# Performance work log

Measured on AMD Instinct MI355X. Metric: run time of the kernel, lower is better.

## Reference

```python
import jax, jax.numpy as jnp
import numpy as np

MAX_SPAN_LEN = 6

def setup_inputs() -> dict:
    key = jax.random.key(0)
    k1, k2 = jax.random.split(key)
    B, L, H = 16, 1024, 768
    span_adjacency = jax.random.uniform(k1, (B, L, L, 1), dtype=jnp.float32)
    bound_hidden = jax.random.normal(k2, (B, L, H), dtype=jnp.float32)
    return {"span_adjacency": span_adjacency, "bound_hidden": bound_hidden}

def reference(span_adjacency, bound_hidden):
    # out[:, j] = sum_{i=j}^{min(j+6,L)-1} w[:,j,i] * concat(h[:,i], h[:,j])
    B, L, H = bound_hidden.shape
    d = jnp.arange(MAX_SPAN_LEN)                      # window offsets [6]
    j = jnp.arange(L)                                  # [L]
    idx = jnp.minimum(j[:, None] + d[None, :], L - 1)  # [L, 6] clamped gather index
    valid = (j[:, None] + d[None, :]) < L              # [L, 6] window mask
    # gather window weights: w[:, j, j+d] -> [B, L, 6]
    w = span_adjacency[:, j[:, None], idx, 0] * valid.astype(span_adjacency.dtype)
    # gather window hiddens: h[:, j+d] -> [B, L, 6, H]
    h_win = bound_hidden[:, idx]
    first = jnp.einsum('bjd,bjdh->bjh', w, h_win)      # sum_i w * h_i
    wsum = jnp.sum(w, axis=-1, keepdims=True)          # [B, L, 1]
    second = bound_hidden * wsum                       # h_j * sum_i w
    return jnp.concatenate([first, second], axis=-1)   # [B, L, 2H]
```

## Files before the change

kernel.cpp:

```cpp
#include <hip/hip_runtime.h>


#define LROWS 1024
#define HDIM  768
#define SPANW 6
#define HALO  (SPANW - 1)
#define RCHUNK 16
#define CHUNKS (LROWS / RCHUNK)
#define BLK   384

typedef float f32x2 __attribute__((ext_vector_type(2)));

__global__ __launch_bounds__(BLK) void boundary_seg_kernel(
    const float* __restrict__ span,
    const float* __restrict__ bound,
    float* __restrict__ out)
{
    const int tid  = threadIdx.x;
    const int b    = blockIdx.x >> 6;
    const int j0   = (blockIdx.x & (CHUNKS - 1)) * RCHUNK;
    const int bL   = b * LROWS;
    const int colf = tid << 1;

    const float* bcol = bound + (size_t)bL * HDIM + colf;
    f32x2 h[RCHUNK + HALO];
#pragma unroll
    for (int r = 0; r < RCHUNK + HALO; ++r) {
        int gr = j0 + r;
        if (gr > LROWS - 1) gr = LROWS - 1;
        h[r] = *(const f32x2*)(bcol + (size_t)gr * HDIM);
    }

    const float* sdiag = span + (size_t)(bL + j0) * LROWS + j0;

#pragma unroll
    for (int s = 0; s < RCHUNK; ++s) {
        const int j = j0 + s;
        const float* sp = sdiag + (size_t)s * (LROWS + 1);

        float w[SPANW], wsum = 0.f;
#pragma unroll
        for (int d = 0; d < SPANW; ++d) {
            w[d] = (j + d < LROWS) ? sp[d] : 0.f;
            wsum += w[d];
        }

        f32x2 acc = w[0] * h[s]     + w[1] * h[s + 1] + w[2] * h[s + 2]
                  + w[3] * h[s + 3] + w[4] * h[s + 4] + w[5] * h[s + 5];
        const f32x2 sec = h[s] * wsum;

        float* orow = out + (size_t)(bL + j) * (2 * HDIM) + colf;
        *(f32x2*)orow          = acc;
        *(f32x2*)(orow + HDIM) = sec;
    }
}

extern "C" void kernel_launch(void* const* d_in, const int* in_sizes, int n_in,
                              void* d_out, int out_size, void* d_ws, size_t ws_size,
                              hipStream_t stream) {
    const float* span  = (const float*)d_in[0];
    const float* bound = (const float*)d_in[1];
    float* out = (float*)d_out;

    const int B = in_sizes[1] / (LROWS * HDIM);
    dim3 grid(B * CHUNKS), block(BLK);
    hipLaunchKernelGGL(boundary_seg_kernel, grid, block, 0, stream,
                       span, bound, out);
}
```

Measured before the change: 180.9 us.

## Widen to float4 columns, stage span weights in LDS, swizzle workgroups across XCDs

Each thread now handles four columns with 128-bit loads and stores, which halves the block size. The six diagonal span weights per row and their sum are loaded once by 16 threads into shared memory instead of by every thread. Workgroup IDs are remapped so that consecutive chunks land on the same XCD, aiming for better L2 locality on the halo rows. The cost is a barrier, a larger register footprint (21 float4 values), and a launch-bounds occupancy hint.

```diff
diff --git a/kernel.cpp b/kernel.cpp
--- a/kernel.cpp
+++ b/kernel.cpp
@@ -7,51 +7,64 @@
 #define HALO  (SPANW - 1)
 #define RCHUNK 16
 #define CHUNKS (LROWS / RCHUNK)
-#define BLK   384
+#define BLK   192
 
-typedef float f32x2 __attribute__((ext_vector_type(2)));
+typedef float f32x4 __attribute__((ext_vector_type(4)));
 
-__global__ __launch_bounds__(BLK) void boundary_seg_kernel(
+__global__ __launch_bounds__(BLK, 4) void boundary_seg_kernel(
     const float* __restrict__ span,
     const float* __restrict__ bound,
     float* __restrict__ out)
 {
-    const int tid  = threadIdx.x;
-    const int b    = blockIdx.x >> 6;
-    const int j0   = (blockIdx.x & (CHUNKS - 1)) * RCHUNK;
+    __shared__ float sw[RCHUNK][8];
+
+    const int tid = threadIdx.x;
+
+    const unsigned nwg = gridDim.x;
+    const unsigned wg  = (nwg & 7u) ? blockIdx.x
+                       : (blockIdx.x & 7u) * (nwg >> 3) + (blockIdx.x >> 3);
+
+    const int b    = wg >> 6;
+    const int j0   = (wg & (CHUNKS - 1)) * RCHUNK;
     const int bL   = b * LROWS;
-    const int colf = tid << 1;
+    const int colf = tid << 2;
 
     const float* bcol = bound + (size_t)bL * HDIM + colf;
-    f32x2 h[RCHUNK + HALO];
+    f32x4 h[RCHUNK + HALO];
 #pragma unroll
     for (int r = 0; r < RCHUNK + HALO; ++r) {
         int gr = j0 + r;
         if (gr > LROWS - 1) gr = LROWS - 1;
-        h[r] = *(const f32x2*)(bcol + (size_t)gr * HDIM);
+        h[r] = *(const f32x4*)(bcol + (size_t)gr * HDIM);
     }
 
-    const float* sdiag = span + (size_t)(bL + j0) * LROWS + j0;
+    if (tid < RCHUNK) {
+        const int j = j0 + tid;
+        const float* sp = span + (size_t)(bL + j) * LROWS + j;
+        float wsum = 0.f;
+#pragma unroll
+        for (int d = 0; d < SPANW; ++d) {
+            const float v = (j + d < LROWS) ? sp[d] : 0.f;
+            sw[tid][d] = v;
+            wsum += v;
+        }
+        sw[tid][6] = wsum;
+        sw[tid][7] = 0.f;
+    }
+    __syncthreads();
 
 #pragma unroll
     for (int s = 0; s < RCHUNK; ++s) {
-        const int j = j0 + s;
-        const float* sp = sdiag + (size_t)s * (LROWS + 1);
+        const f32x4 w0 = *(const f32x4*)&sw[s][0];
+        const f32x4 w1 = *(const f32x4*)&sw[s][4];
 
-        float w[SPANW], wsum = 0.f;
-#pragma unroll
-        for (int d = 0; d < SPANW; ++d) {
-            w[d] = (j + d < LROWS) ? sp[d] : 0.f;
-            wsum += w[d];
-        }
+        f32x4 acc = w0[0] * h[s]     + w0[1] * h[s + 1] + w0[2] * h[s + 2]
+                  + w0[3] * h[s + 3] + w1[0] * h[s + 4] + w1[1] * h[s + 5];
+        const f32x4 sec = h[s] * w1[2];
 
-        f32x2 acc = w[0] * h[s]     + w[1] * h[s + 1] + w[2] * h[s + 2]
-                  + w[3] * h[s + 3] + w[4] * h[s + 4] + w[5] * h[s + 5];
-        const f32x2 sec = h[s] * wsum;
-
-        float* orow = out + (size_t)(bL + j) * (2 * HDIM) + colf;
-        *(f32x2*)orow          = acc;
-        *(f32x2*)(orow + HDIM) = sec;
+        float* orow = out + (size_t)(bL + j0 + s) * (2 * HDIM) + colf;
+        *(f32x4*)orow          = acc;
+        *(f32x4*)(orow + HDIM) = sec;
     }
 }
 
```

Result: faster. 175.4 us (-3.0%).
